# Optimization experiments

Measured on AMD Instinct MI355X. Metric: run time of the kernel, lower is better.

The kernel has to match this reference:

```python
import jax, jax.numpy as jnp
import numpy as np
from jax import lax

# dims: batch, seq, d_model, d_inner, d_state, dt_rank, conv_k, fno_modes, n_inner_blocks, d_model_out
B_, L_, D_, DI_, N_, R_, K_, M_, NB_, DOUT_ = 2, 256, 256, 512, 32, 16, 4, 16, 7, 76416
EPS = 1e-5


def setup_inputs() -> dict:
    key = jax.random.key(0)
    ks = iter(jax.random.split(key, 48))
    nrm = lambda shape, s=0.02: jax.random.normal(next(ks), shape, jnp.float32) * s
    a_log = jnp.log(jnp.arange(1, N_ + 1, dtype=jnp.float32))  # Mamba S4D-real init
    return {
        "x": jax.random.normal(next(ks), (B_, L_, D_), jnp.float32),
        "ln_w": jnp.ones((NB_, D_), jnp.float32), "ln_b": jnp.zeros((NB_, D_), jnp.float32),
        "in_w": nrm((NB_, 2 * DI_, D_)),
        "conv_w": nrm((NB_, DI_, K_)), "conv_b": jnp.zeros((NB_, DI_), jnp.float32),
        "xproj_w": nrm((NB_, R_ + N_, DI_)),
        "dt_w": nrm((NB_, DI_, R_)), "dt_b": jnp.full((NB_, DI_), -4.0, jnp.float32),
        "A_log": jnp.broadcast_to(a_log, (NB_, DI_, N_)),
        "Cmat": nrm((NB_, DI_, N_)), "Dvec": jnp.ones((NB_, DI_), jnp.float32),
        "spec_r": nrm((NB_, DI_, M_)), "spec_i": nrm((NB_, DI_, M_)),
        "out_w": nrm((NB_, D_, DI_)),
        "fln_w": jnp.ones((D_,), jnp.float32), "fln_b": jnp.zeros((D_,), jnp.float32),
        "f_in_w": nrm((2 * DI_, D_)),
        "f_conv_w": nrm((DI_, K_)), "f_conv_b": jnp.zeros((DI_,), jnp.float32),
        "f_xproj_w": nrm((R_ + N_, DI_)),
        "f_dt_w": nrm((DI_, R_)), "f_dt_b": jnp.full((DI_,), -4.0, jnp.float32),
        "f_A_log": jnp.broadcast_to(a_log, (DI_, N_)),
        "f_Cmat": nrm((DI_, N_)), "f_Dvec": jnp.ones((DI_,), jnp.float32),
        "f_spec_r": nrm((DI_, M_)), "f_spec_i": nrm((DI_, M_)),
        "f_out_w": nrm((DOUT_, DI_)),
    }


def _silu(v):
    return v * jax.nn.sigmoid(v)


def _layernorm(v, w, b):
    mu = v.mean(-1, keepdims=True)
    var = ((v - mu) ** 2).mean(-1, keepdims=True)
    return (v - mu) * lax.rsqrt(var + EPS) * w + b


def _mixer(h, in_w, conv_w, conv_b, xproj_w, dt_w, dt_b, A_log, Cmat, Dvec, spec_r, spec_i, out_w):
    # MambawithfixedC_time: selective scan with learned fixed C + 1D FNO spectral branch
    B, L, _ = h.shape
    Di, K = conv_w.shape
    R = dt_w.shape[1]
    x, z = jnp.split(h @ in_w.T, 2, axis=-1)                      # (B,L,Di) each
    # causal depthwise conv along sequence
    xc = jnp.pad(x.transpose(0, 2, 1), ((0, 0), (0, 0), (K - 1, 0)))  # (B,Di,L+K-1)
    x = lax.conv_general_dilated(xc, conv_w[:, None, :], (1,), 'VALID',
                                 feature_group_count=Di)          # (B,Di,L)
    x = _silu(x.transpose(0, 2, 1) + conv_b)                      # (B,L,Di)
    dbl = x @ xproj_w.T                                           # (B,L,R+N)
    dt = jax.nn.softplus(dbl[..., :R] @ dt_w.T + dt_b)            # (B,L,Di)
    Bmat = dbl[..., R:]                                           # (B,L,N)
    A = -jnp.exp(A_log)                                           # (Di,N)
    dA = jnp.exp(dt[..., None] * A)                               # (B,L,Di,N)
    dBx = dt[..., None] * Bmat[:, :, None, :] * x[..., None]      # (B,L,Di,N)

    def step(hstate, inputs):
        a_t, bx_t = inputs
        hstate = a_t * hstate + bx_t
        return hstate, jnp.einsum('bdn,dn->bd', hstate, Cmat)

    h0 = jnp.zeros((B, Di, A.shape[1]), x.dtype)
    _, y = lax.scan(step, h0, (dA.transpose(1, 0, 2, 3), dBx.transpose(1, 0, 2, 3)))
    y = y.transpose(1, 0, 2) + Dvec * x                           # (B,L,Di)
    # FNO spectral branch: keep first M rFFT modes over sequence axis
    M = spec_r.shape[1]
    Xf = jnp.fft.rfft(x, axis=1)[:, :M, :]                        # (B,M,Di) complex
    W = (spec_r + 1j * spec_i).T                                  # (M,Di)
    y = y + jnp.fft.irfft(Xf * W, n=L, axis=1)
    return (y * _silu(z)) @ out_w.T


def reference(x, ln_w, ln_b, in_w, conv_w, conv_b, xproj_w, dt_w, dt_b, A_log, Cmat,
              Dvec, spec_r, spec_i, out_w, fln_w, fln_b, f_in_w, f_conv_w, f_conv_b,
              f_xproj_w, f_dt_w, f_dt_b, f_A_log, f_Cmat, f_Dvec, f_spec_r, f_spec_i,
              f_out_w):
    hidden, residual = x, None
    for i in range(ln_w.shape[0]):  # inner Blocks (prenorm residual + mixer)
        residual = hidden if residual is None else residual + hidden
        hidden = _layernorm(residual, ln_w[i], ln_b[i])
        hidden = _mixer(hidden, in_w[i], conv_w[i], conv_b[i], xproj_w[i], dt_w[i],
                        dt_b[i], A_log[i], Cmat[i], Dvec[i], spec_r[i], spec_i[i], out_w[i])
    # finalBlock: residual add + norm + mixer projecting to d_model_out
    residual = residual + hidden
    hidden = _layernorm(residual, fln_w, fln_b)
    return _mixer(hidden, f_in_w, f_conv_w, f_conv_b, f_xproj_w, f_dt_w, f_dt_b,
                  f_A_log, f_Cmat, f_Dvec, f_spec_r, f_spec_i, f_out_w)
```

## Files before the change

kernel.cpp:

```cpp
#include <hip/hip_runtime.h>
#include <hip/hip_bf16.h>

#define BLr 512
#define Dm 256
#define DIc 512
#define DOUTc 76416

typedef short bf16x8 __attribute__((ext_vector_type(8)));
typedef float f32x16 __attribute__((ext_vector_type(16)));

__device__ __forceinline__ unsigned short f2bf(float f){
  unsigned u = __builtin_bit_cast(unsigned, f);
  u += 0x7FFFu + ((u >> 16) & 1u);
  return (unsigned short)(u >> 16);
}

__device__ __forceinline__ void gl_lds16(const void* g, void* l){
  __builtin_amdgcn_global_load_lds(
      (const __attribute__((address_space(1))) unsigned int*)g,
      (__attribute__((address_space(3))) unsigned int*)l, 16, 0, 0);
}

__device__ __forceinline__ bf16x8 cvt8(float4 a, float4 b){
  unsigned q0 = (unsigned)f2bf(a.x) | ((unsigned)f2bf(a.y) << 16);
  unsigned q1 = (unsigned)f2bf(a.z) | ((unsigned)f2bf(a.w) << 16);
  unsigned q2 = (unsigned)f2bf(b.x) | ((unsigned)f2bf(b.y) << 16);
  unsigned q3 = (unsigned)f2bf(b.z) | ((unsigned)f2bf(b.w) << 16);
  uint4 u{q0, q1, q2, q3};
  return __builtin_bit_cast(bf16x8, u);
}

__global__ void init_resid_kernel(float* __restrict__ resid, const float* __restrict__ x){
  int i = blockIdx.x*256 + threadIdx.x;
  resid[i] = x[i];
}

__global__ __launch_bounds__(256) void ln_inproj_kernel(
    float* __restrict__ xz, const float* __restrict__ resid,
    const float* __restrict__ lw, const float* __restrict__ lb,
    const float* __restrict__ iw)
{
  __shared__ __align__(16) float Aln[32][260];
  __shared__ __align__(16) float Wf[64*256];
  const int tid = threadIdx.x;
  const int m0 = blockIdx.y*32, n0 = blockIdx.x*64;
  const int wv = tid>>6, lane = tid&63;
  #pragma unroll
  for (int i = 0; i < 16; ++i){
    int col = i*4 + wv;
    int sc  = lane ^ (col&7);
    gl_lds16(iw + (size_t)(n0+col)*256 + sc*4, (void*)((char*)Wf + col*1024));
  }
  float4 w4 = *(const float4*)(lw + lane*4);
  float4 b4 = *(const float4*)(lb + lane*4);
  #pragma unroll
  for (int rr = 0; rr < 8; ++rr){
    int row = wv*8 + rr;
    float4 v = *(const float4*)(resid + (m0+row)*Dm + lane*4);
    float s  = v.x+v.y+v.z+v.w;
    float s2 = v.x*v.x+v.y*v.y+v.z*v.z+v.w*v.w;
    #pragma unroll
    for (int m = 1; m < 64; m <<= 1){ s += __shfl_xor(s,m); s2 += __shfl_xor(s2,m); }
    float mu = s*(1.f/256.f), var = s2*(1.f/256.f) - mu*mu;
    float rs = rsqrtf(var + 1e-5f);
    float4 o;
    o.x = (v.x-mu)*rs*w4.x + b4.x;
    o.y = (v.y-mu)*rs*w4.y + b4.y;
    o.z = (v.z-mu)*rs*w4.z + b4.z;
    o.w = (v.w-mu)*rs*w4.w + b4.w;
    *(float4*)&Aln[row][lane*4] = o;
  }
  __syncthreads();
  const int ty = tid>>4, tx = tid&15;
  float acc[2][4] = {{0,0,0,0},{0,0,0,0}};
  #pragma unroll 4
  for (int kk = 0; kk < 64; ++kk){
    float4 a0 = *(const float4*)&Aln[ty][kk*4];
    float4 a1 = *(const float4*)&Aln[ty+16][kk*4];
    #pragma unroll
    for (int j = 0; j < 4; ++j){
      int col = tx + 16*j;
      float4 w = *(const float4*)&Wf[(col*64 + (kk ^ (col&7)))*4];
      acc[0][j] += a0.x*w.x + a0.y*w.y + a0.z*w.z + a0.w*w.w;
      acc[1][j] += a1.x*w.x + a1.y*w.y + a1.z*w.z + a1.w*w.w;
    }
  }
  #pragma unroll
  for (int j = 0; j < 4; ++j){
    xz[(m0+ty)*1024    + n0 + tx + 16*j] = acc[0][j];
    xz[(m0+ty+16)*1024 + n0 + tx + 16*j] = acc[1][j];
  }
}

__global__ __launch_bounds__(256) void conv_xproj_dt_kernel(
    float* __restrict__ xc, float* __restrict__ dbl, float* __restrict__ dtv,
    const float* __restrict__ xz, const float* __restrict__ cw,
    const float* __restrict__ cb, const float* __restrict__ xw,
    const float* __restrict__ dw, const float* __restrict__ db)
{
  __shared__ __align__(16) float xcr[512];
  __shared__ float dblq[16];
  const int row = blockIdx.x, tid = threadIdx.x;
  const int t = row & 255;
  #pragma unroll
  for (int h = 0; h < 2; ++h){
    int d = tid + h*256;
    float4 w = *(const float4*)(cw + d*4);
    float acc = cb[d];
    const float* xp = xz + (size_t)row*1024 + d;
    if (t >= 3) acc += w.x*xp[-3072] + w.y*xp[-2048] + w.z*xp[-1024] + w.w*xp[0];
    else {
      acc += w.w*xp[0];
      if (t >= 1) acc += w.z*xp[-1024];
      if (t >= 2) acc += w.y*xp[-2048];
    }
    float v = acc / (1.f + __expf(-acc));
    xcr[d] = v;
    xc[row*DIc + d] = v;
  }
  __syncthreads();
  const int wv = tid>>6, lane = tid&63;
  float4 xa = *(const float4*)&xcr[lane*4];
  float4 xb = *(const float4*)&xcr[256 + lane*4];
  for (int o = 0; o < 12; ++o){
    int oo = wv*12 + o;
    const float* wr = xw + oo*DIc;
    float4 wa = *(const float4*)(wr + lane*4);
    float4 wb = *(const float4*)(wr + 256 + lane*4);
    float p = xa.x*wa.x + xa.y*wa.y + xa.z*wa.z + xa.w*wa.w
            + xb.x*wb.x + xb.y*wb.y + xb.z*wb.z + xb.w*wb.w;
    #pragma unroll
    for (int m = 1; m < 64; m <<= 1) p += __shfl_xor(p, m);
    if (lane == 0){
      dbl[row*48 + oo] = p;
      if (oo < 16) dblq[oo] = p;
    }
  }
  __syncthreads();
  #pragma unroll
  for (int h = 0; h < 2; ++h){
    int d = tid + h*256;
    const float4* wr = (const float4*)(dw + d*16);
    float4 w0 = wr[0], w1 = wr[1], w2 = wr[2], w3 = wr[3];
    float acc = db[d];
    acc += dblq[0]*w0.x  + dblq[1]*w0.y  + dblq[2]*w0.z  + dblq[3]*w0.w;
    acc += dblq[4]*w1.x  + dblq[5]*w1.y  + dblq[6]*w1.z  + dblq[7]*w1.w;
    acc += dblq[8]*w2.x  + dblq[9]*w2.y  + dblq[10]*w2.z + dblq[11]*w2.w;
    acc += dblq[12]*w3.x + dblq[13]*w3.y + dblq[14]*w3.z + dblq[15]*w3.w;
    dtv[row*DIc + d] = (acc > 20.f) ? acc : log1pf(__expf(acc));
  }
}

__global__ __launch_bounds__(128) void scan_fft_gate_kernel(
    float* __restrict__ g, unsigned short* __restrict__ gbf,
    const float* __restrict__ xc, const float* __restrict__ dtv,
    const float* __restrict__ dbl, const float* __restrict__ xz,
    const float* __restrict__ A_log, const float* __restrict__ Cmat,
    const float* __restrict__ Dvec, const float* __restrict__ sr,
    const float* __restrict__ si)
{
  __shared__ float xs[4][260], dts[4][260], ys[4][260];
  __shared__ float Bs[256][33];
  __shared__ float ct[256], st[256];
  __shared__ float Ysr[4][17], Ysi[4][17];
  __shared__ float Pl[2][2][32][67];
  const int tid = threadIdx.x;
  const int b = blockIdx.y, d0 = blockIdx.x*4;
  #pragma unroll
  for (int k = 0; k < 2; ++k){
    int idx = tid + k*128;
    float sv, cv;
    __sincosf((float)idx * 0.02454369260617026f, &sv, &cv);
    ct[idx] = cv; st[idx] = sv;
  }
  const int dd = tid & 3, tq = tid >> 2;
  #pragma unroll
  for (int i = 0; i < 8; ++i){
    int t = i*32 + tq;
    xs[dd][t]  = xc [(b*256+t)*DIc + d0+dd];
    dts[dd][t] = dtv[(b*256+t)*DIc + d0+dd];
  }
  {
    int n = tid & 31, tb = tid >> 5;
    #pragma unroll 8
    for (int i = 0; i < 64; ++i){
      int t = i*4 + tb;
      Bs[t][n] = dbl[(b*256+t)*48 + 16 + n];
    }
  }
  __syncthreads();
  const int wv = tid>>6, lane = tid&63;
  {
    const int ch2 = lane>>5;
    const int ddw = wv*2 + ch2;
    const int d = d0 + ddw;
    const int n = lane & 31;
    const int tloc = lane & 31;
    const float A  = -__expf(A_log[d*32+n]);
    const float Cv = Cmat[d*32+n];
    float h = 0.f;
    for (int pass = 0; pass < 4; ++pass){
      #pragma unroll 4
      for (int i = 0; i < 64; ++i){
        int t = pass*64 + i;
        float dtl = dts[ddw][t];
        float xv  = xs[ddw][t];
        float Bv  = Bs[t][n];
        h = __expf(dtl*A)*h + dtl*Bv*xv;
        Pl[wv][ch2][n][i] = h*Cv;
      }
      float s0 = 0.f, s1 = 0.f;
      #pragma unroll 8
      for (int n2 = 0; n2 < 32; ++n2){
        s0 += Pl[wv][ch2][n2][tloc];
        s1 += Pl[wv][ch2][n2][32+tloc];
      }
      ys[ddw][pass*64 + tloc]      = s0;
      ys[ddw][pass*64 + 32 + tloc] = s1;
    }
  }
  {
    const int ddw = wv*2 + (lane>>5);
    const int m = lane & 15, im = (lane>>4) & 1;
    float acc = 0.f;
    for (int t = 0; t < 256; ++t){
      int idx = (m*t) & 255;
      acc += xs[ddw][t] * (im ? st[idx] : ct[idx]);
    }
    float other = __shfl_xor(acc, 16);
    const int d = d0 + ddw;
    float wr = sr[d*16+m], wi = si[d*16+m];
    if (im == 0){
      float Xr = acc, Xi = -other;
      Ysr[ddw][m] = Xr*wr - Xi*wi;
    } else {
      float Xi = -acc, Xr = other;
      Ysi[ddw][m] = Xr*wi + Xi*wr;
    }
  }
  __syncthreads();
  {
    const float Dv = Dvec[d0+dd];
    float yr[16], yi[16];
    #pragma unroll
    for (int m = 0; m < 16; ++m){ yr[m] = Ysr[dd][m]; yi[m] = Ysi[dd][m]; }
    #pragma unroll 2
    for (int i = 0; i < 8; ++i){
      int t = i*32 + tq;
      float fv = 0.5f * yr[0];
      #pragma unroll
      for (int m = 1; m < 16; ++m){
        int idx = (m*t) & 255;
        fv += yr[m]*ct[idx] - yi[m]*st[idx];
      }
      float yv = ys[dd][t] + Dv*xs[dd][t] + fv*0.0078125f;
      float z = xz[(b*256+t)*1024 + 512 + d0+dd];
      float gv = yv * (z / (1.f + __expf(-z)));
      int oi = (b*256+t)*DIc + d0+dd;
      g[oi] = gv;
      gbf[oi] = f2bf(gv);
    }
  }
}

__global__ __launch_bounds__(256) void outproj_resid_kernel(
    float* __restrict__ resid, const float* __restrict__ g, const float* __restrict__ ow)
{
  __shared__ __align__(16) float As[32][36];
  __shared__ __align__(16) float Ws2[16][36];
  const int tid = threadIdx.x;
  const int n0 = blockIdx.x*16, m0 = blockIdx.y*32;
  const int r = tid>>3, c8 = (tid&7)*4;
  const int ty = tid>>4, tx = tid&15;
  float a00=0, a10=0;
  for (int kc = 0; kc < 512; kc += 32){
    __syncthreads();
    *(float4*)&As[r][c8] = *(const float4*)(g + (m0+r)*DIc + kc + c8);
    if (tid < 128){
      *(float4*)&Ws2[tid>>3][c8] = *(const float4*)(ow + (n0+(tid>>3))*DIc + kc + c8);
    }
    __syncthreads();
    #pragma unroll
    for (int kk = 0; kk < 8; ++kk){
      float4 a0 = *(const float4*)&As[ty][kk*4];
      float4 a1 = *(const float4*)&As[ty+16][kk*4];
      float4 w0 = *(const float4*)&Ws2[tx][kk*4];
      a00 += a0.x*w0.x + a0.y*w0.y + a0.z*w0.z + a0.w*w0.w;
      a10 += a1.x*w0.x + a1.y*w0.y + a1.z*w0.z + a1.w*w0.w;
    }
  }
  resid[(m0+ty)*Dm    + n0+tx] += a00;
  resid[(m0+ty+16)*Dm + n0+tx] += a10;
}

__global__ __launch_bounds__(512) void gemm_final2_kernel(
    float* __restrict__ Out, const unsigned short* __restrict__ Gb,
    const float* __restrict__ W)
{
  __shared__ __align__(16) unsigned short As[32768];
  __shared__ __align__(16) unsigned short Wb[4096];
  const int tid = threadIdx.x;
  const int wv = tid>>6, lane = tid&63;
  const int half = lane>>5, lm = lane&31;
  const int nq = wv & 1, mq = wv >> 1;
  const int col = blockIdx.x*64 + nq*32 + lm;
  const int wcol = tid>>3, wkq = tid&7;
  const float* Wsrc = W + (size_t)(blockIdx.x*64 + wcol)*512 + wkq*8;
  unsigned short* Wdst = Wb + (wcol*8 + (wkq ^ (wcol&7)))*8;
  f32x16 acc[4];
  #pragma unroll
  for (int i = 0; i < 4; ++i)
    #pragma unroll
    for (int rg = 0; rg < 16; ++rg) acc[i][rg] = 0.f;

  for (int k0 = 0; k0 < 512; k0 += 64){
    float4 wf0 = *(const float4*)(Wsrc + k0);
    float4 wf1 = *(const float4*)(Wsrc + k0 + 4);
    #pragma unroll
    for (int p = 0; p < 8; ++p){
      int R  = p*64 + wv*8;
      int rr = R + (lane>>3);
      int cg = (lane&7) ^ (rr&7);
      gl_lds16(Gb + rr*512 + k0 + cg*8, (void*)((char*)As + R*128));
    }
    *(bf16x8*)Wdst = cvt8(wf0, wf1);
    __syncthreads();
    #pragma unroll
    for (int j = 0; j < 4; ++j){
      const int c = j*2 + half;
      bf16x8 bv = *(const bf16x8*)(Wb + (((nq*32+lm)*8) + (c ^ ((nq*32+lm)&7)))*8);
      #pragma unroll
      for (int mt = 0; mt < 4; ++mt){
        int rr = mq*128 + mt*32 + lm;
        bf16x8 av = *(const bf16x8*)((const char*)As + (rr*8 + (c ^ (rr&7)))*16);
        acc[mt] = __builtin_amdgcn_mfma_f32_32x32x16_bf16(av, bv, acc[mt], 0, 0, 0);
      }
    }
    __syncthreads();
  }
  #pragma unroll
  for (int mt = 0; mt < 4; ++mt){
    int rbase = mq*128 + mt*32 + 4*half;
    #pragma unroll
    for (int rg = 0; rg < 16; ++rg){
      int row = rbase + (rg&3) + 8*(rg>>2);
      Out[(size_t)row*DOUTc + col] = acc[mt][rg];
    }
  }
}

extern "C" void kernel_launch(void* const* d_in, const int* in_sizes, int n_in,
                              void* d_out, int out_size, void* d_ws, size_t ws_size,
                              hipStream_t stream)
{
  (void)in_sizes; (void)n_in; (void)out_size; (void)ws_size;
  const float* x       = (const float*)d_in[0];
  const float* ln_w    = (const float*)d_in[1];
  const float* ln_b    = (const float*)d_in[2];
  const float* in_w    = (const float*)d_in[3];
  const float* conv_w  = (const float*)d_in[4];
  const float* conv_b  = (const float*)d_in[5];
  const float* xproj_w = (const float*)d_in[6];
  const float* dt_w    = (const float*)d_in[7];
  const float* dt_b    = (const float*)d_in[8];
  const float* A_log   = (const float*)d_in[9];
  const float* Cmat    = (const float*)d_in[10];
  const float* Dvec    = (const float*)d_in[11];
  const float* spec_r  = (const float*)d_in[12];
  const float* spec_i  = (const float*)d_in[13];
  const float* out_w   = (const float*)d_in[14];
  const float* fln_w   = (const float*)d_in[15];
  const float* fln_b   = (const float*)d_in[16];
  const float* f_in_w  = (const float*)d_in[17];
  const float* f_conv_w= (const float*)d_in[18];
  const float* f_conv_b= (const float*)d_in[19];
  const float* f_xproj = (const float*)d_in[20];
  const float* f_dt_w  = (const float*)d_in[21];
  const float* f_dt_b  = (const float*)d_in[22];
  const float* f_A_log = (const float*)d_in[23];
  const float* f_Cmat  = (const float*)d_in[24];
  const float* f_Dvec  = (const float*)d_in[25];
  const float* f_spec_r= (const float*)d_in[26];
  const float* f_spec_i= (const float*)d_in[27];
  const float* f_out_w = (const float*)d_in[28];

  float* ws   = (float*)d_ws;
  float* resid = ws;
  float* xz    = ws + 131072;
  float* xcb   = ws + 655360;
  float* dblb  = ws + 917504;
  float* dtb   = ws + 942080;
  float* gb    = ws + 1204224;
  unsigned short* g_bf = (unsigned short*)(ws + 1466368);
  float* outp = (float*)d_out;

  init_resid_kernel<<<512, 256, 0, stream>>>(resid, x);

  for (int i = 0; i < 8; ++i){
    const bool fin = (i == 7);
    const float* lw = fin ? fln_w   : ln_w    + i*256;
    const float* lb = fin ? fln_b   : ln_b    + i*256;
    const float* iw = fin ? f_in_w  : in_w    + i*262144;
    const float* cw = fin ? f_conv_w: conv_w  + i*2048;
    const float* cb = fin ? f_conv_b: conv_b  + i*512;
    const float* xw = fin ? f_xproj : xproj_w + i*24576;
    const float* dw = fin ? f_dt_w  : dt_w    + i*8192;
    const float* db = fin ? f_dt_b  : dt_b    + i*512;
    const float* al = fin ? f_A_log : A_log   + i*16384;
    const float* cm = fin ? f_Cmat  : Cmat    + i*16384;
    const float* dv = fin ? f_Dvec  : Dvec    + i*512;
    const float* sr = fin ? f_spec_r: spec_r  + i*8192;
    const float* si = fin ? f_spec_i: spec_i  + i*8192;

    ln_inproj_kernel<<<dim3(16, 16), 256, 0, stream>>>(xz, resid, lw, lb, iw);
    conv_xproj_dt_kernel<<<512, 256, 0, stream>>>(xcb, dblb, dtb, xz, cw, cb, xw, dw, db);
    scan_fft_gate_kernel<<<dim3(128, 2), 128, 0, stream>>>(gb, g_bf, xcb, dtb, dblb, xz,
                                                           al, cm, dv, sr, si);
    if (!fin){
      outproj_resid_kernel<<<dim3(16, 16), 256, 0, stream>>>(resid, gb, out_w + i*131072);
    } else {
      gemm_final2_kernel<<<DOUTc/64, 512, 0, stream>>>(outp, g_bf, f_out_w);
    }
  }
}
```

Measured before the change: 952.5 us.

## Split scan and FFT across warps, restage outproj GEMM, drop residual init kernel

The scan/FFT/gate kernel now runs 256 threads, with two waves doing the selective scan while the other two compute the spectral DFT concurrently. The B operand is read directly from global memory instead of being staged in shared memory. The out-projection kernel now loads its weight tile once via direct-to-LDS async loads with XOR swizzling, processes K in 128-wide chunks, and reads the residual base from x on the first block. This removes the separate residual-init launch. Reading B from global inside the serial scan loop adds latency to the critical path.

Result: faster. 844.9 us (-11.3%).

```diff
diff --git a/kernel.cpp b/kernel.cpp
--- a/kernel.cpp
+++ b/kernel.cpp
@@ -30,13 +30,8 @@
   return __builtin_bit_cast(bf16x8, u);
 }
 
-__global__ void init_resid_kernel(float* __restrict__ resid, const float* __restrict__ x){
-  int i = blockIdx.x*256 + threadIdx.x;
-  resid[i] = x[i];
-}
-
 __global__ __launch_bounds__(256) void ln_inproj_kernel(
-    float* __restrict__ xz, const float* __restrict__ resid,
+    float* __restrict__ xz, const float* __restrict__ src,
     const float* __restrict__ lw, const float* __restrict__ lb,
     const float* __restrict__ iw)
 {
@@ -56,7 +51,7 @@
   #pragma unroll
   for (int rr = 0; rr < 8; ++rr){
     int row = wv*8 + rr;
-    float4 v = *(const float4*)(resid + (m0+row)*Dm + lane*4);
+    float4 v = *(const float4*)(src + (m0+row)*Dm + lane*4);
     float s  = v.x+v.y+v.z+v.w;
     float s2 = v.x*v.x+v.y*v.y+v.z*v.z+v.w*v.w;
     #pragma unroll
@@ -122,6 +117,7 @@
   const int wv = tid>>6, lane = tid&63;
   float4 xa = *(const float4*)&xcr[lane*4];
   float4 xb = *(const float4*)&xcr[256 + lane*4];
+  #pragma unroll
   for (int o = 0; o < 12; ++o){
     int oo = wv*12 + o;
     const float* wr = xw + oo*DIc;
@@ -151,7 +147,7 @@
   }
 }
 
-__global__ __launch_bounds__(128) void scan_fft_gate_kernel(
+__global__ __launch_bounds__(256) void scan_fft_gate_kernel(
     float* __restrict__ g, unsigned short* __restrict__ gbf,
     const float* __restrict__ xc, const float* __restrict__ dtv,
     const float* __restrict__ dbl, const float* __restrict__ xz,
@@ -160,37 +156,26 @@
     const float* __restrict__ si)
 {
   __shared__ float xs[4][260], dts[4][260], ys[4][260];
-  __shared__ float Bs[256][33];
   __shared__ float ct[256], st[256];
   __shared__ float Ysr[4][17], Ysi[4][17];
-  __shared__ float Pl[2][2][32][67];
+  __shared__ float Pl[2][2][32][65];
   const int tid = threadIdx.x;
   const int b = blockIdx.y, d0 = blockIdx.x*4;
-  #pragma unroll
-  for (int k = 0; k < 2; ++k){
-    int idx = tid + k*128;
+  {
     float sv, cv;
-    __sincosf((float)idx * 0.02454369260617026f, &sv, &cv);
-    ct[idx] = cv; st[idx] = sv;
+    __sincosf((float)tid * 0.02454369260617026f, &sv, &cv);
+    ct[tid] = cv; st[tid] = sv;
   }
   const int dd = tid & 3, tq = tid >> 2;
   #pragma unroll
-  for (int i = 0; i < 8; ++i){
-    int t = i*32 + tq;
+  for (int i = 0; i < 4; ++i){
+    int t = i*64 + tq;
     xs[dd][t]  = xc [(b*256+t)*DIc + d0+dd];
     dts[dd][t] = dtv[(b*256+t)*DIc + d0+dd];
   }
-  {
-    int n = tid & 31, tb = tid >> 5;
-    #pragma unroll 8
-    for (int i = 0; i < 64; ++i){
-      int t = i*4 + tb;
-      Bs[t][n] = dbl[(b*256+t)*48 + 16 + n];
-    }
-  }
   __syncthreads();
   const int wv = tid>>6, lane = tid&63;
-  {
+  if (wv < 2){
     const int ch2 = lane>>5;
     const int ddw = wv*2 + ch2;
     const int d = d0 + ddw;
@@ -198,14 +183,15 @@
     const int tloc = lane & 31;
     const float A  = -__expf(A_log[d*32+n]);
     const float Cv = Cmat[d*32+n];
+    const float* Bp = dbl + (size_t)(b*256)*48 + 16 + n;
     float h = 0.f;
     for (int pass = 0; pass < 4; ++pass){
-      #pragma unroll 4
+      #pragma unroll 8
       for (int i = 0; i < 64; ++i){
         int t = pass*64 + i;
         float dtl = dts[ddw][t];
         float xv  = xs[ddw][t];
-        float Bv  = Bs[t][n];
+        float Bv  = Bp[t*48];
         h = __expf(dtl*A)*h + dtl*Bv*xv;
         Pl[wv][ch2][n][i] = h*Cv;
       }
@@ -218,9 +204,8 @@
       ys[ddw][pass*64 + tloc]      = s0;
       ys[ddw][pass*64 + 32 + tloc] = s1;
     }
-  }
-  {
-    const int ddw = wv*2 + (lane>>5);
+  } else {
+    const int ddw = (wv-2)*2 + (lane>>5);
     const int m = lane & 15, im = (lane>>4) & 1;
     float acc = 0.f;
     for (int t = 0; t < 256; ++t){
@@ -245,8 +230,8 @@
     #pragma unroll
     for (int m = 0; m < 16; ++m){ yr[m] = Ysr[dd][m]; yi[m] = Ysi[dd][m]; }
     #pragma unroll 2
-    for (int i = 0; i < 8; ++i){
-      int t = i*32 + tq;
+    for (int i = 0; i < 4; ++i){
+      int t = i*64 + tq;
       float fv = 0.5f * yr[0];
       #pragma unroll
       for (int m = 1; m < 16; ++m){
@@ -264,33 +249,53 @@
 }
 
 __global__ __launch_bounds__(256) void outproj_resid_kernel(
-    float* __restrict__ resid, const float* __restrict__ g, const float* __restrict__ ow)
-{
-  __shared__ __align__(16) float As[32][36];
-  __shared__ __align__(16) float Ws2[16][36];
+    float* __restrict__ resid, const float* __restrict__ base,
+    const float* __restrict__ g, const float* __restrict__ ow)
+{
+  __shared__ __align__(16) float Ws2[16*512];
+  __shared__ __align__(16) float As[32*128];
   const int tid = threadIdx.x;
+  const int wv = tid>>6, lane = tid&63;
   const int n0 = blockIdx.x*16, m0 = blockIdx.y*32;
-  const int r = tid>>3, c8 = (tid&7)*4;
   const int ty = tid>>4, tx = tid&15;
-  float a00=0, a10=0;
-  for (int kc = 0; kc < 512; kc += 32){
+  #pragma unroll
+  for (int i = 0; i < 4; ++i){
+    int row = wv*4 + i;
+    #pragma unroll
+    for (int h = 0; h < 2; ++h){
+      int c = h*64 + lane;
+      int s = c ^ (row&7);
+      gl_lds16(ow + (size_t)(n0+row)*DIc + s*4,
+               (void*)((char*)Ws2 + row*2048 + h*1024));
+    }
+  }
+  float b0 = base[(m0+ty)*Dm + n0+tx];
+  float b1 = base[(m0+ty+16)*Dm + n0+tx];
+  float a00 = 0.f, a10 = 0.f;
+  for (int kc = 0; kc < 512; kc += 128){
+    if (kc) __syncthreads();
+    #pragma unroll
+    for (int j = 0; j < 4; ++j){
+      int R = wv*8 + j*2;
+      int r = R + (lane>>5);
+      int c = lane&31;
+      int s = c ^ (r&7);
+      gl_lds16(g + (size_t)(m0+r)*DIc + kc + s*4,
+               (void*)((char*)As + R*512));
+    }
     __syncthreads();
-    *(float4*)&As[r][c8] = *(const float4*)(g + (m0+r)*DIc + kc + c8);
-    if (tid < 128){
-      *(float4*)&Ws2[tid>>3][c8] = *(const float4*)(ow + (n0+(tid>>3))*DIc + kc + c8);
-    }
-    __syncthreads();
-    #pragma unroll
-    for (int kk = 0; kk < 8; ++kk){
-      float4 a0 = *(const float4*)&As[ty][kk*4];
-      float4 a1 = *(const float4*)&As[ty+16][kk*4];
-      float4 w0 = *(const float4*)&Ws2[tx][kk*4];
+    const int kb = kc>>2;
+    #pragma unroll
+    for (int kk = 0; kk < 32; ++kk){
+      float4 a0 = *(const float4*)((const char*)As + ty*512      + ((kk ^ (ty&7))<<4));
+      float4 a1 = *(const float4*)((const char*)As + (ty+16)*512 + ((kk ^ (ty&7))<<4));
+      float4 w0 = *(const float4*)((const char*)Ws2 + tx*2048 + (((kb+kk) ^ (tx&7))<<4));
       a00 += a0.x*w0.x + a0.y*w0.y + a0.z*w0.z + a0.w*w0.w;
       a10 += a1.x*w0.x + a1.y*w0.y + a1.z*w0.z + a1.w*w0.w;
     }
   }
-  resid[(m0+ty)*Dm    + n0+tx] += a00;
-  resid[(m0+ty+16)*Dm + n0+tx] += a10;
+  resid[(m0+ty)*Dm    + n0+tx] = b0 + a00;
+  resid[(m0+ty+16)*Dm + n0+tx] = b1 + a10;
 }
 
 __global__ __launch_bounds__(512) void gemm_final2_kernel(
@@ -394,8 +399,6 @@
   unsigned short* g_bf = (unsigned short*)(ws + 1466368);
   float* outp = (float*)d_out;
 
-  init_resid_kernel<<<512, 256, 0, stream>>>(resid, x);
-
   for (int i = 0; i < 8; ++i){
     const bool fin = (i == 7);
     const float* lw = fin ? fln_w   : ln_w    + i*256;
@@ -412,12 +415,14 @@
     const float* sr = fin ? f_spec_r: spec_r  + i*8192;
     const float* si = fin ? f_spec_i: spec_i  + i*8192;
 
-    ln_inproj_kernel<<<dim3(16, 16), 256, 0, stream>>>(xz, resid, lw, lb, iw);
+    const float* src = (i == 0) ? x : resid;
+    ln_inproj_kernel<<<dim3(16, 16), 256, 0, stream>>>(xz, src, lw, lb, iw);
     conv_xproj_dt_kernel<<<512, 256, 0, stream>>>(xcb, dblb, dtb, xz, cw, cb, xw, dw, db);
-    scan_fft_gate_kernel<<<dim3(128, 2), 128, 0, stream>>>(gb, g_bf, xcb, dtb, dblb, xz,
+    scan_fft_gate_kernel<<<dim3(128, 2), 256, 0, stream>>>(gb, g_bf, xcb, dtb, dblb, xz,
                                                            al, cm, dv, sr, si);
     if (!fin){
-      outproj_resid_kernel<<<dim3(16, 16), 256, 0, stream>>>(resid, gb, out_w + i*131072);
+      outproj_resid_kernel<<<dim3(16, 16), 256, 0, stream>>>(resid, (i == 0) ? x : resid,
+                                                             gb, out_w + i*131072);
     } else {
       gemm_final2_kernel<<<DOUTc/64, 512, 0, stream>>>(outp, g_bf, f_out_w);
     }
```
